# Performance work log

Hardware: AMD Instinct MI355X
Metric: run time of the kernel (lower is better)

The kernel has to match this reference:

```python
import jax, jax.numpy as jnp
import numpy as np

B, C, H, W = 8, 512, 32, 32
HEADS = 8
GROUPS = 32
EPS = 1e-5


def setup_inputs() -> dict:
    key = jax.random.key(0)
    ks = jax.random.split(key, 7)
    x = jax.random.normal(ks[0], (B, C, H, W), dtype=jnp.float32)
    gamma = jnp.ones((C,), dtype=jnp.float32)
    beta = jnp.zeros((C,), dtype=jnp.float32)
    w_qkv = jax.random.normal(ks[1], (3 * C, C), dtype=jnp.float32) * 0.02
    b_qkv = jnp.zeros((3 * C,), dtype=jnp.float32)
    # NOTE: original zero-inits proj; we use small random weights so the
    # attention path contributes to the output (zero proj => out == x).
    w_proj = jax.random.normal(ks[2], (C, C), dtype=jnp.float32) * 0.02
    b_proj = jnp.zeros((C,), dtype=jnp.float32)
    return {"x": x, "gamma": gamma, "beta": beta, "w_qkv": w_qkv,
            "b_qkv": b_qkv, "w_proj": w_proj, "b_proj": b_proj}


def group_norm(x, gamma, beta):
    b, c, h, w = x.shape
    xg = x.reshape(b, GROUPS, -1)
    mu = xg.mean(axis=-1, keepdims=True)
    var = xg.var(axis=-1, keepdims=True)
    xn = ((xg - mu) * jax.lax.rsqrt(var + EPS)).reshape(b, c, h, w)
    return xn * gamma[:, None, None] + beta[:, None, None]


def reference(x, gamma, beta, w_qkv, b_qkv, w_proj, b_proj):
    b, c, h, w = x.shape
    hd = c // HEADS
    n = h * w
    hn = group_norm(x, gamma, beta).reshape(b, c, n)        # [B,C,N]
    # 1x1 conv == channel matmul
    qkv = jnp.einsum('oc,bcn->bon', w_qkv, hn) + b_qkv[:, None]
    qkv = qkv.reshape(b, 3, HEADS, hd, n)
    q, k, v = qkv[:, 0], qkv[:, 1], qkv[:, 2]               # [B,H,hd,N]
    scale = hd ** -0.5
    scores = jnp.einsum('bhci,bhcj->bhij', q, k) * scale    # [B,H,N,N]
    attn = jax.nn.softmax(scores, axis=-1)                  # stable (max-sub)
    out = jnp.einsum('bhij,bhcj->bhci', attn, v).reshape(b, c, n)
    proj = jnp.einsum('oc,bcn->bon', w_proj, out) + b_proj[:, None]
    return x + proj.reshape(b, c, h, w)
```

## Files before the change

### kernel.cpp

```cpp
#include <hip/hip_runtime.h>
#include <hip/hip_cooperative_groups.h>
#include <math.h>

namespace cg = cooperative_groups;

#define Bn 8
#define Cc 512
#define HW 1024
#define HEADS 8
#define HD 64
#define GROUPS 32
#define CPG 16
#define EPS 1e-5f

typedef float f32x4 __attribute__((ext_vector_type(4)));
typedef __bf16 bf16x8 __attribute__((ext_vector_type(8)));
typedef __bf16 bf16x4 __attribute__((ext_vector_type(4)));
typedef short s16x4 __attribute__((ext_vector_type(4)));
typedef unsigned u32x2 __attribute__((ext_vector_type(2)));

__device__ __forceinline__ void async16(const __bf16* g, __bf16* l) {
    __builtin_amdgcn_global_load_lds((const __attribute__((address_space(1))) unsigned int*)g,
                                     (__attribute__((address_space(3))) unsigned int*)l, 16, 0, 0);
}

__device__ __forceinline__ f32x4 mfma16(bf16x4 a, bf16x4 b, f32x4 c) {
    return __builtin_amdgcn_mfma_f32_16x16x16bf16_1k(
        __builtin_bit_cast(s16x4, a), __builtin_bit_cast(s16x4, b), c, 0, 0, 0);
}

__device__ __forceinline__ unsigned pk_bf16(float f1, float f0) {
    return __builtin_amdgcn_perm(__builtin_bit_cast(unsigned, f1),
                                 __builtin_bit_cast(unsigned, f0), 0x07060302u);
}

__device__ __forceinline__ void gn_phase(char* smem, int blk, int tid,
    const float* __restrict__ x, const float* __restrict__ gamma,
    const float* __restrict__ beta, __bf16* __restrict__ hnT,
    const float* __restrict__ wq, __bf16* __restrict__ wq_bf,
    const float* __restrict__ wp, __bf16* __restrict__ wp_bf) {
    if (blk >= 256) {
        int base = (blk - 256) * 512 + tid;
        #pragma unroll
        for (int u = 0; u < 2; ++u) {
            int i = base + u * 256;
            if (i < 196608) {
                float4 v = ((const float4*)wq)[i];
                bf16x4 o = { (__bf16)v.x, (__bf16)v.y, (__bf16)v.z, (__bf16)v.w };
                ((bf16x4*)wq_bf)[i] = o;
            } else {
                int j = i - 196608;
                float4 v = ((const float4*)wp)[j];
                bf16x4 o = { (__bf16)v.x, (__bf16)v.y, (__bf16)v.z, (__bf16)v.w };
                ((bf16x4*)wp_bf)[j] = o;
            }
        }
        return;
    }
    __bf16* xs = (__bf16*)smem;
    float* fs = (float*)smem;
    int b = blk >> 5, g = blk & 31;
    const float* xp = x + ((size_t)b * Cc + g * CPG) * HW;

    float s = 0.f, ss = 0.f;
    for (int i4 = tid; i4 < 4096; i4 += 256) {
        float4 v = ((const float4*)xp)[i4];
        s  += (v.x + v.y) + (v.z + v.w);
        ss += (v.x * v.x + v.y * v.y) + (v.z * v.z + v.w * v.w);
        bf16x4 o = { (__bf16)v.x, (__bf16)v.y, (__bf16)v.z, (__bf16)v.w };
        ((bf16x4*)xs)[i4] = o;
    }
    for (int off = 32; off > 0; off >>= 1) {
        s  += __shfl_down(s, off);
        ss += __shfl_down(ss, off);
    }
    int wave = tid >> 6, lane = tid & 63;
    __syncthreads();
    float keep = 0.f;
    if (tid < 20) keep = (float)xs[tid];
    __syncthreads();
    if (lane == 0) { fs[wave * 2] = s; fs[wave * 2 + 1] = ss; }
    __syncthreads();
    if (tid == 0) {
        float S  = fs[0] + fs[2] + fs[4] + fs[6];
        float SS = fs[1] + fs[3] + fs[5] + fs[7];
        float mean = S / 16384.f;
        float var  = SS / 16384.f - mean * mean;
        fs[8] = mean;
        fs[9] = rsqrtf(var + EPS);
    }
    __syncthreads();
    float mean = fs[8], rstd = fs[9];
    __syncthreads();
    if (tid < 20) xs[tid] = (__bf16)keep;
    __syncthreads();

    float gl[16], bl[16];
    #pragma unroll
    for (int c = 0; c < 16; ++c) { gl[c] = gamma[g * CPG + c]; bl[c] = beta[g * CPG + c]; }
    #pragma unroll
    for (int u = 0; u < 4; ++u) {
        int n = tid + u * 256;
        union { __bf16 bs[16]; uint4 q[2]; } o;
        #pragma unroll
        for (int c = 0; c < 16; ++c) {
            float v = (float)xs[c * 1024 + n];
            o.bs[c] = (__bf16)((v - mean) * rstd * gl[c] + bl[c]);
        }
        uint4* dst = (uint4*)(hnT + ((size_t)b * HW + n) * Cc + g * CPG);
        dst[0] = o.q[0];
        dst[1] = o.q[1];
    }
}

__device__ __forceinline__ void qkv_tile(char* smem, int t, int tid,
    const __bf16* __restrict__ hnT, const __bf16* __restrict__ wq,
    const float* __restrict__ bias, __bf16* __restrict__ qkT,
    __bf16* __restrict__ vbuf, float scaleLo) {
    __bf16* As = (__bf16*)smem;
    __bf16* Bs = (__bf16*)(smem + 16384);
    int wv = tid >> 6, lane = tid & 63, ln = lane & 15, quad = lane >> 4;
    int b = t / 96, rem = t % 96;
    int y = rem >> 3, xv = rem & 7;
    bool isQK = y < 8;
    int bm = (isQK ? y : y - 8) * 128;
    int bn = xv * 128;
    const __bf16* hb = hnT + (size_t)b * HW * Cc;
    const __bf16* Pb = isQK ? hb : wq + (size_t)1024 * 512;
    const __bf16* Qb = isQK ? wq : hb;
    int wm = (wv >> 1) * 64, wn = (wv & 1) * 64;

    f32x4 acc[4][4];
    #pragma unroll
    for (int i = 0; i < 4; ++i)
        #pragma unroll
        for (int j = 0; j < 4; ++j) acc[i][j] = (f32x4){0.f, 0.f, 0.f, 0.f};

    for (int k0 = 0; k0 < 512; k0 += 64) {
        __syncthreads();
        #pragma unroll
        for (int u = 0; u < 4; ++u) {
            int idx = u * 256 + tid;
            int r = idx >> 3, lc = idx & 7;
            int cg2 = lc ^ (r & 7);
            async16(Pb + (size_t)(bm + r) * 512 + k0 + cg2 * 8, &As[r * 64 + lc * 8]);
            async16(Qb + (size_t)(bn + r) * 512 + k0 + cg2 * 8, &Bs[r * 64 + lc * 8]);
        }
        __syncthreads();
        bf16x8 af[4][2], bff[4][2];
        #pragma unroll
        for (int mt = 0; mt < 4; ++mt) {
            int row = wm + mt * 16 + ln;
            #pragma unroll
            for (int h = 0; h < 2; ++h) {
                int cc = (h * 4 + quad) ^ (ln & 7);
                af[mt][h] = *(const bf16x8*)&As[row * 64 + cc * 8];
            }
        }
        #pragma unroll
        for (int nt = 0; nt < 4; ++nt) {
            int row = wn + nt * 16 + ln;
            #pragma unroll
            for (int h = 0; h < 2; ++h) {
                int cc = (h * 4 + quad) ^ (ln & 7);
                bff[nt][h] = *(const bf16x8*)&Bs[row * 64 + cc * 8];
            }
        }
        #pragma unroll
        for (int mt = 0; mt < 4; ++mt)
            #pragma unroll
            for (int nt = 0; nt < 4; ++nt) {
                acc[mt][nt] = __builtin_amdgcn_mfma_f32_16x16x32_bf16(af[mt][0], bff[nt][0], acc[mt][nt], 0, 0, 0);
                acc[mt][nt] = __builtin_amdgcn_mfma_f32_16x16x32_bf16(af[mt][1], bff[nt][1], acc[mt][nt], 0, 0, 0);
            }
    }

    if (isQK) {
        __bf16* out = qkT + (size_t)b * HW * 1024;
        float bcol[4], scol[4];
        #pragma unroll
        for (int nt = 0; nt < 4; ++nt) {
            int col = bn + wn + nt * 16 + ln;
            bcol[nt] = bias[col];
            scol[nt] = (col < 512) ? scaleLo : 1.0f;
        }
        #pragma unroll
        for (int mt = 0; mt < 4; ++mt)
            #pragma unroll
            for (int r = 0; r < 4; ++r) {
                int row = bm + wm + mt * 16 + quad * 4 + r;
                #pragma unroll
                for (int nt = 0; nt < 4; ++nt) {
                    int col = bn + wn + nt * 16 + ln;
                    out[(size_t)row * 1024 + col] = (__bf16)((acc[mt][nt][r] + bcol[nt]) * scol[nt]);
                }
            }
    } else {
        __bf16* out = vbuf + (size_t)b * Cc * HW;
        #pragma unroll
        for (int mt = 0; mt < 4; ++mt)
            #pragma unroll
            for (int r = 0; r < 4; ++r) {
                int row = bm + wm + mt * 16 + quad * 4 + r;
                float brow = bias[1024 + row];
                #pragma unroll
                for (int nt = 0; nt < 4; ++nt) {
                    int col = bn + wn + nt * 16 + ln;
                    out[(size_t)row * 1024 + col] = (__bf16)(acc[mt][nt][r] + brow);
                }
            }
    }
}

__device__ __forceinline__ void attn_unit(char* smem, int blk, int tid,
    const __bf16* __restrict__ qkT, const __bf16* __restrict__ vbuf,
    __bf16* __restrict__ attnT) {
    __bf16* Ks = (__bf16*)smem;
    __bf16* Vs = (__bf16*)(smem + 16384);
    int wv = tid >> 6, lane = tid & 63, ln = lane & 15, quad = lane >> 4;
    int h = blk & 7, qb = (blk >> 3) & 7, b = blk >> 6;
    int i0 = qb * 128 + wv * 32;

    const __bf16* qbase = qkT + ((size_t)b * HW + i0 + ln) * 1024 + h * HD + quad * 8;
    bf16x8 qf[2][2];
    #pragma unroll
    for (int mt = 0; mt < 2; ++mt) {
        qf[mt][0] = *(const bf16x8*)(qbase + (size_t)mt * 16 * 1024);
        qf[mt][1] = *(const bf16x8*)(qbase + (size_t)mt * 16 * 1024 + 32);
    }

    f32x4 oacc[2][4];
    #pragma unroll
    for (int mt = 0; mt < 2; ++mt)
        #pragma unroll
        for (int ct = 0; ct < 4; ++ct) oacc[mt][ct] = (f32x4){0.f, 0.f, 0.f, 0.f};
    float lsum[2] = {0.f, 0.f};

    for (int kt = 0; kt < 8; ++kt) {
        __syncthreads();
        #pragma unroll
        for (int hh = 0; hh < 2; ++hh) {
            int kb = kt * 128 + hh * 64;
            #pragma unroll
            for (int u = 0; u < 2; ++u) {
                int idx = u * 256 + tid;
                int r = idx >> 3, lc = idx & 7;
                int cg2 = lc ^ (r & 7);
                async16(qkT + ((size_t)b * HW + kb + r) * 1024 + 512 + h * HD + cg2 * 8,
                        &Ks[hh * 4096 + idx * 8]);
                async16(vbuf + ((size_t)b * Cc + h * HD + r) * HW + kb + cg2 * 8,
                        &Vs[hh * 4096 + idx * 8]);
            }
        }
        __syncthreads();

        #pragma unroll
        for (int hh = 0; hh < 2; ++hh) {
            f32x4 st[2][4];
            #pragma unroll
            for (int jt = 0; jt < 4; ++jt) {
                int row = jt * 16 + ln;
                int c0 = quad ^ (ln & 7);
                int c1 = (4 + quad) ^ (ln & 7);
                bf16x8 kf0 = *(const bf16x8*)&Ks[hh * 4096 + row * 64 + c0 * 8];
                bf16x8 kf1 = *(const bf16x8*)&Ks[hh * 4096 + row * 64 + c1 * 8];
                #pragma unroll
                for (int mt = 0; mt < 2; ++mt) {
                    f32x4 s = (f32x4){0.f, 0.f, 0.f, 0.f};
                    s = __builtin_amdgcn_mfma_f32_16x16x32_bf16(kf0, qf[mt][0], s, 0, 0, 0);
                    s = __builtin_amdgcn_mfma_f32_16x16x32_bf16(kf1, qf[mt][1], s, 0, 0, 0);
                    st[mt][jt] = s;
                }
            }

            bf16x4 pk[2][4];
            #pragma unroll
            for (int mt = 0; mt < 2; ++mt)
                #pragma unroll
                for (int jt = 0; jt < 4; ++jt) {
                    float p0 = __builtin_amdgcn_exp2f(st[mt][jt][0]);
                    float p1 = __builtin_amdgcn_exp2f(st[mt][jt][1]);
                    float p2 = __builtin_amdgcn_exp2f(st[mt][jt][2]);
                    float p3 = __builtin_amdgcn_exp2f(st[mt][jt][3]);
                    lsum[mt] += (p0 + p1) + (p2 + p3);
                    u32x2 w = { pk_bf16(p1, p0), pk_bf16(p3, p2) };
                    pk[mt][jt] = __builtin_bit_cast(bf16x4, w);
                }

            #pragma unroll
            for (int ct = 0; ct < 4; ++ct) {
                int row = ct * 16 + ln;
                bf16x4 vf[4];
                #pragma unroll
                for (int kss = 0; kss < 4; ++kss) {
                    int cc16 = (kss * 2 + (quad >> 1)) ^ (ln & 7);
                    vf[kss] = *(const bf16x4*)&Vs[hh * 4096 + row * 64 + cc16 * 8 + (quad & 1) * 4];
                }
                #pragma unroll
                for (int mt = 0; mt < 2; ++mt)
                    #pragma unroll
                    for (int kss = 0; kss < 4; ++kss)
                        oacc[mt][ct] = mfma16(vf[kss], pk[mt][kss], oacc[mt][ct]);
            }
        }
    }

    #pragma unroll
    for (int mt = 0; mt < 2; ++mt) {
        lsum[mt] += __shfl_xor(lsum[mt], 16);
        lsum[mt] += __shfl_xor(lsum[mt], 32);
        float rl = 1.f / lsum[mt];
        __bf16* op = attnT + ((size_t)b * HW + i0 + mt * 16 + ln) * Cc + h * HD + quad * 4;
        #pragma unroll
        for (int ct = 0; ct < 4; ++ct) {
            bf16x4 o = { (__bf16)(oacc[mt][ct][0] * rl), (__bf16)(oacc[mt][ct][1] * rl),
                         (__bf16)(oacc[mt][ct][2] * rl), (__bf16)(oacc[mt][ct][3] * rl) };
            *(bf16x4*)(op + ct * 16) = o;
        }
    }
}

__device__ __forceinline__ void proj_unit(char* smem, int blk, int tid,
    const __bf16* __restrict__ wp, const __bf16* __restrict__ attnT,
    const float* __restrict__ bias, const float* __restrict__ resid,
    float* __restrict__ outp) {
    __bf16* As = (__bf16*)smem;
    __bf16* Bs = (__bf16*)(smem + 8192);
    int wv = tid >> 6, lane = tid & 63, ln = lane & 15, quad = lane >> 4;
    int xv = blk & 7, y = (blk >> 3) & 7, b = blk >> 6;
    int bm = y * 64, bn = xv * 128;
    const __bf16* Qb = attnT + (size_t)b * HW * Cc;
    int wm = (wv >> 1) * 32, wn = (wv & 1) * 64;

    f32x4 acc[2][4];
    #pragma unroll
    for (int i = 0; i < 2; ++i)
        #pragma unroll
        for (int j = 0; j < 4; ++j) acc[i][j] = (f32x4){0.f, 0.f, 0.f, 0.f};

    for (int k0 = 0; k0 < 512; k0 += 64) {
        __syncthreads();
        #pragma unroll
        for (int u = 0; u < 2; ++u) {
            int idx = u * 256 + tid;
            int r = idx >> 3, lc = idx & 7;
            int cg2 = lc ^ (r & 7);
            async16(wp + (size_t)(bm + r) * 512 + k0 + cg2 * 8, &As[r * 64 + lc * 8]);
        }
        #pragma unroll
        for (int u = 0; u < 4; ++u) {
            int idx = u * 256 + tid;
            int r = idx >> 3, lc = idx & 7;
            int cg2 = lc ^ (r & 7);
            async16(Qb + (size_t)(bn + r) * 512 + k0 + cg2 * 8, &Bs[r * 64 + lc * 8]);
        }
        __syncthreads();
        bf16x8 af[2][2], bff[4][2];
        #pragma unroll
        for (int mt = 0; mt < 2; ++mt) {
            int row = wm + mt * 16 + ln;
            #pragma unroll
            for (int h = 0; h < 2; ++h) {
                int cc = (h * 4 + quad) ^ (ln & 7);
                af[mt][h] = *(const bf16x8*)&As[row * 64 + cc * 8];
            }
        }
        #pragma unroll
        for (int nt = 0; nt < 4; ++nt) {
            int row = wn + nt * 16 + ln;
            #pragma unroll
            for (int h = 0; h < 2; ++h) {
                int cc = (h * 4 + quad) ^ (ln & 7);
                bff[nt][h] = *(const bf16x8*)&Bs[row * 64 + cc * 8];
            }
        }
        #pragma unroll
        for (int mt = 0; mt < 2; ++mt)
            #pragma unroll
            for (int nt = 0; nt < 4; ++nt) {
                acc[mt][nt] = __builtin_amdgcn_mfma_f32_16x16x32_bf16(af[mt][0], bff[nt][0], acc[mt][nt], 0, 0, 0);
                acc[mt][nt] = __builtin_amdgcn_mfma_f32_16x16x32_bf16(af[mt][1], bff[nt][1], acc[mt][nt], 0, 0, 0);
            }
    }

    float* out = outp + (size_t)b * Cc * HW;
    const float* res = resid + (size_t)b * Cc * HW;
    #pragma unroll
    for (int mt = 0; mt < 2; ++mt)
        #pragma unroll
        for (int r = 0; r < 4; ++r) {
            int row = bm + wm + mt * 16 + quad * 4 + r;
            float bv = bias[row];
            #pragma unroll
            for (int nt = 0; nt < 4; ++nt) {
                int col = bn + wn + nt * 16 + ln;
                size_t idx = (size_t)row * 1024 + col;
                out[idx] = acc[mt][nt][r] + bv + res[idx];
            }
        }
}

__global__ __launch_bounds__(256, 3) void mega(
    const float* __restrict__ x, const float* __restrict__ gamma,
    const float* __restrict__ beta,
    const float* __restrict__ wq_f, const float* __restrict__ wp_f,
    const float* __restrict__ bq, const float* __restrict__ bp,
    __bf16* wq_bf, __bf16* wp_bf, __bf16* hnT, __bf16* qkT,
    __bf16* vbuf, __bf16* attnT, float* out, float qscale) {
    __shared__ __align__(16) char smem[32768];
    int blk = blockIdx.x, tid = threadIdx.x;
    cg::grid_group grid = cg::this_grid();

    gn_phase(smem, blk, tid, x, gamma, beta, hnT, wq_f, wq_bf, wp_f, wp_bf);
    grid.sync();
    qkv_tile(smem, blk, tid, hnT, wq_bf, bq, qkT, vbuf, qscale);
    grid.sync();
    if (blk < 512) attn_unit(smem, blk, tid, qkT, vbuf, attnT);
    grid.sync();
    if (blk < 512) proj_unit(smem, blk, tid, wp_bf, attnT, bp, x, out);
}

__global__ __launch_bounds__(256, 3) void gn_k(
    const float* x, const float* gamma, const float* beta, __bf16* hnT,
    const float* wq, __bf16* wq_bf, const float* wp, __bf16* wp_bf) {
    __shared__ __align__(16) char smem[32768];
    gn_phase(smem, blockIdx.x, threadIdx.x, x, gamma, beta, hnT, wq, wq_bf, wp, wp_bf);
}
__global__ __launch_bounds__(256, 3) void qkv_k(
    const __bf16* hnT, const __bf16* wq, const float* bq,
    __bf16* qkT, __bf16* vbuf, float qscale) {
    __shared__ __align__(16) char smem[32768];
    qkv_tile(smem, blockIdx.x, threadIdx.x, hnT, wq, bq, qkT, vbuf, qscale);
}
__global__ __launch_bounds__(256, 3) void attn_k(
    const __bf16* qkT, const __bf16* vbuf, __bf16* attnT) {
    __shared__ __align__(16) char smem[32768];
    attn_unit(smem, blockIdx.x, threadIdx.x, qkT, vbuf, attnT);
}
__global__ __launch_bounds__(256, 3) void proj_k(
    const __bf16* wp, const __bf16* attnT, const float* bp,
    const float* resid, float* out) {
    __shared__ __align__(16) char smem[32768];
    proj_unit(smem, blockIdx.x, threadIdx.x, wp, attnT, bp, resid, out);
}

extern "C" void kernel_launch(void* const* d_in, const int* in_sizes, int n_in,
                              void* d_out, int out_size, void* d_ws, size_t ws_size,
                              hipStream_t stream) {
    const float* x      = (const float*)d_in[0];
    const float* gamma  = (const float*)d_in[1];
    const float* beta   = (const float*)d_in[2];
    const float* w_qkv  = (const float*)d_in[3];
    const float* b_qkv  = (const float*)d_in[4];
    const float* w_proj = (const float*)d_in[5];
    const float* b_proj = (const float*)d_in[6];
    float* out = (float*)d_out;

    __bf16* wq_bf  = (__bf16*)d_ws;
    __bf16* wp_bf  = wq_bf + (size_t)1536 * 512;
    __bf16* hnT    = wp_bf + (size_t)512 * 512;
    __bf16* qkT    = hnT + (size_t)Bn * HW * Cc;
    __bf16* vbuf   = qkT + (size_t)Bn * HW * 1024;
    __bf16* attnT  = vbuf + (size_t)Bn * Cc * HW;

    float qscale = 0.125f * 1.44269504088896f;

    gn_k<<<768, 256, 0, stream>>>(x, gamma, beta, hnT, w_qkv, wq_bf, w_proj, wp_bf);
    qkv_k<<<768, 256, 0, stream>>>(hnT, wq_bf, b_qkv, qkT, vbuf, qscale);
    attn_k<<<512, 256, 0, stream>>>(qkT, vbuf, attnT);
    proj_k<<<512, 256, 0, stream>>>(wp_bf, attnT, b_proj, x, out);
}
```

Measured before the change: 141.3 us.

## Double-buffer LDS tiles in qkv, attention and projection kernels; drop cooperative mega kernel

Adds a two-stage LDS ping-pong to the qkv, attention and projection loops. The async global-to-LDS copy of the next K tile is issued before the MFMA work on the current tile, which should hide load latency and halves the barriers per iteration. Shared memory per block doubles (64KB/48KB) and launch bounds drop to 2 blocks per CU, trading occupancy for overlap. The unused cooperative mega kernel is removed.

```diff
diff --git a/kernel.cpp b/kernel.cpp
--- a/kernel.cpp
+++ b/kernel.cpp
@@ -1,8 +1,5 @@
 #include <hip/hip_runtime.h>
-#include <hip/hip_cooperative_groups.h>
 #include <math.h>
-
-namespace cg = cooperative_groups;
 
 #define Bn 8
 #define Cc 512
@@ -113,12 +110,25 @@
     }
 }
 
+__device__ __forceinline__ void qkv_stage(char* base, int tid,
+    const __bf16* __restrict__ Pb, const __bf16* __restrict__ Qb,
+    int bm, int bn, int k0) {
+    __bf16* As = (__bf16*)base;
+    __bf16* Bs = (__bf16*)(base + 16384);
+    #pragma unroll
+    for (int u = 0; u < 4; ++u) {
+        int idx = u * 256 + tid;
+        int r = idx >> 3, lc = idx & 7;
+        int cg2 = lc ^ (r & 7);
+        async16(Pb + (size_t)(bm + r) * 512 + k0 + cg2 * 8, &As[idx * 8]);
+        async16(Qb + (size_t)(bn + r) * 512 + k0 + cg2 * 8, &Bs[idx * 8]);
+    }
+}
+
 __device__ __forceinline__ void qkv_tile(char* smem, int t, int tid,
     const __bf16* __restrict__ hnT, const __bf16* __restrict__ wq,
     const float* __restrict__ bias, __bf16* __restrict__ qkT,
     __bf16* __restrict__ vbuf, float scaleLo) {
-    __bf16* As = (__bf16*)smem;
-    __bf16* Bs = (__bf16*)(smem + 16384);
     int wv = tid >> 6, lane = tid & 63, ln = lane & 15, quad = lane >> 4;
     int b = t / 96, rem = t % 96;
     int y = rem >> 3, xv = rem & 7;
@@ -136,17 +146,16 @@
         #pragma unroll
         for (int j = 0; j < 4; ++j) acc[i][j] = (f32x4){0.f, 0.f, 0.f, 0.f};
 
-    for (int k0 = 0; k0 < 512; k0 += 64) {
-        __syncthreads();
-        #pragma unroll
-        for (int u = 0; u < 4; ++u) {
-            int idx = u * 256 + tid;
-            int r = idx >> 3, lc = idx & 7;
-            int cg2 = lc ^ (r & 7);
-            async16(Pb + (size_t)(bm + r) * 512 + k0 + cg2 * 8, &As[r * 64 + lc * 8]);
-            async16(Qb + (size_t)(bn + r) * 512 + k0 + cg2 * 8, &Bs[r * 64 + lc * 8]);
-        }
-        __syncthreads();
+    char* sm_cur = smem;
+    char* sm_nxt = smem + 32768;
+
+    qkv_stage(sm_cur, tid, Pb, Qb, bm, bn, 0);
+    __syncthreads();
+
+    for (int kt = 0; kt < 8; ++kt) {
+        if (kt < 7) qkv_stage(sm_nxt, tid, Pb, Qb, bm, bn, (kt + 1) * 64);
+        __bf16* As = (__bf16*)sm_cur;
+        __bf16* Bs = (__bf16*)(sm_cur + 16384);
         bf16x8 af[4][2], bff[4][2];
         #pragma unroll
         for (int mt = 0; mt < 4; ++mt) {
@@ -173,6 +182,8 @@
                 acc[mt][nt] = __builtin_amdgcn_mfma_f32_16x16x32_bf16(af[mt][0], bff[nt][0], acc[mt][nt], 0, 0, 0);
                 acc[mt][nt] = __builtin_amdgcn_mfma_f32_16x16x32_bf16(af[mt][1], bff[nt][1], acc[mt][nt], 0, 0, 0);
             }
+        __syncthreads();
+        char* tmp = sm_cur; sm_cur = sm_nxt; sm_nxt = tmp;
     }
 
     if (isQK) {
@@ -212,11 +223,30 @@
     }
 }
 
+__device__ __forceinline__ void attn_stage(char* base, int tid,
+    const __bf16* __restrict__ qkT, const __bf16* __restrict__ vbuf,
+    int b, int h, int kt) {
+    __bf16* Ks = (__bf16*)base;
+    __bf16* Vs = (__bf16*)(base + 16384);
+    #pragma unroll
+    for (int hh = 0; hh < 2; ++hh) {
+        int kb = kt * 128 + hh * 64;
+        #pragma unroll
+        for (int u = 0; u < 2; ++u) {
+            int idx = u * 256 + tid;
+            int r = idx >> 3, lc = idx & 7;
+            int cg2 = lc ^ (r & 7);
+            async16(qkT + ((size_t)b * HW + kb + r) * 1024 + 512 + h * HD + cg2 * 8,
+                    &Ks[hh * 4096 + idx * 8]);
+            async16(vbuf + ((size_t)b * Cc + h * HD + r) * HW + kb + cg2 * 8,
+                    &Vs[hh * 4096 + idx * 8]);
+        }
+    }
+}
+
 __device__ __forceinline__ void attn_unit(char* smem, int blk, int tid,
     const __bf16* __restrict__ qkT, const __bf16* __restrict__ vbuf,
     __bf16* __restrict__ attnT) {
-    __bf16* Ks = (__bf16*)smem;
-    __bf16* Vs = (__bf16*)(smem + 16384);
     int wv = tid >> 6, lane = tid & 63, ln = lane & 15, quad = lane >> 4;
     int h = blk & 7, qb = (blk >> 3) & 7, b = blk >> 6;
     int i0 = qb * 128 + wv * 32;
@@ -236,23 +266,15 @@
         for (int ct = 0; ct < 4; ++ct) oacc[mt][ct] = (f32x4){0.f, 0.f, 0.f, 0.f};
     float lsum[2] = {0.f, 0.f};
 
+    char* sm_cur = smem;
+    char* sm_nxt = smem + 32768;
+    attn_stage(sm_cur, tid, qkT, vbuf, b, h, 0);
+    __syncthreads();
+
     for (int kt = 0; kt < 8; ++kt) {
-        __syncthreads();
-        #pragma unroll
-        for (int hh = 0; hh < 2; ++hh) {
-            int kb = kt * 128 + hh * 64;
-            #pragma unroll
-            for (int u = 0; u < 2; ++u) {
-                int idx = u * 256 + tid;
-                int r = idx >> 3, lc = idx & 7;
-                int cg2 = lc ^ (r & 7);
-                async16(qkT + ((size_t)b * HW + kb + r) * 1024 + 512 + h * HD + cg2 * 8,
-                        &Ks[hh * 4096 + idx * 8]);
-                async16(vbuf + ((size_t)b * Cc + h * HD + r) * HW + kb + cg2 * 8,
-                        &Vs[hh * 4096 + idx * 8]);
-            }
-        }
-        __syncthreads();
+        if (kt < 7) attn_stage(sm_nxt, tid, qkT, vbuf, b, h, kt + 1);
+        __bf16* Ks = (__bf16*)sm_cur;
+        __bf16* Vs = (__bf16*)(sm_cur + 16384);
 
         #pragma unroll
         for (int hh = 0; hh < 2; ++hh) {
@@ -303,6 +325,8 @@
                         oacc[mt][ct] = mfma16(vf[kss], pk[mt][kss], oacc[mt][ct]);
             }
         }
+        __syncthreads();
+        char* tmp = sm_cur; sm_cur = sm_nxt; sm_nxt = tmp;
     }
 
     #pragma unroll
@@ -320,12 +344,31 @@
     }
 }
 
+__device__ __forceinline__ void proj_stage(char* base, int tid,
+    const __bf16* __restrict__ wp, const __bf16* __restrict__ Qb,
+    int bm, int bn, int k0) {
+    __bf16* As = (__bf16*)base;
+    __bf16* Bs = (__bf16*)(base + 8192);
+    #pragma unroll
+    for (int u = 0; u < 2; ++u) {
+        int idx = u * 256 + tid;
+        int r = idx >> 3, lc = idx & 7;
+        int cg2 = lc ^ (r & 7);
+        async16(wp + (size_t)(bm + r) * 512 + k0 + cg2 * 8, &As[idx * 8]);
+    }
+    #pragma unroll
+    for (int u = 0; u < 4; ++u) {
+        int idx = u * 256 + tid;
+        int r = idx >> 3, lc = idx & 7;
+        int cg2 = lc ^ (r & 7);
+        async16(Qb + (size_t)(bn + r) * 512 + k0 + cg2 * 8, &Bs[idx * 8]);
+    }
+}
+
 __device__ __forceinline__ void proj_unit(char* smem, int blk, int tid,
     const __bf16* __restrict__ wp, const __bf16* __restrict__ attnT,
     const float* __restrict__ bias, const float* __restrict__ resid,
     float* __restrict__ outp) {
-    __bf16* As = (__bf16*)smem;
-    __bf16* Bs = (__bf16*)(smem + 8192);
     int wv = tid >> 6, lane = tid & 63, ln = lane & 15, quad = lane >> 4;
     int xv = blk & 7, y = (blk >> 3) & 7, b = blk >> 6;
     int bm = y * 64, bn = xv * 128;
@@ -338,23 +381,15 @@
         #pragma unroll
         for (int j = 0; j < 4; ++j) acc[i][j] = (f32x4){0.f, 0.f, 0.f, 0.f};
 
-    for (int k0 = 0; k0 < 512; k0 += 64) {
-        __syncthreads();
-        #pragma unroll
-        for (int u = 0; u < 2; ++u) {
-            int idx = u * 256 + tid;
-            int r = idx >> 3, lc = idx & 7;
-            int cg2 = lc ^ (r & 7);
-            async16(wp + (size_t)(bm + r) * 512 + k0 + cg2 * 8, &As[r * 64 + lc * 8]);
-        }
-        #pragma unroll
-        for (int u = 0; u < 4; ++u) {
-            int idx = u * 256 + tid;
-            int r = idx >> 3, lc = idx & 7;
-            int cg2 = lc ^ (r & 7);
-            async16(Qb + (size_t)(bn + r) * 512 + k0 + cg2 * 8, &Bs[r * 64 + lc * 8]);
-        }
-        __syncthreads();
+    char* sm_cur = smem;
+    char* sm_nxt = smem + 24576;
+    proj_stage(sm_cur, tid, wp, Qb, bm, bn, 0);
+    __syncthreads();
+
+    for (int kt = 0; kt < 8; ++kt) {
+        if (kt < 7) proj_stage(sm_nxt, tid, wp, Qb, bm, bn, (kt + 1) * 64);
+        __bf16* As = (__bf16*)sm_cur;
+        __bf16* Bs = (__bf16*)(sm_cur + 8192);
         bf16x8 af[2][2], bff[4][2];
         #pragma unroll
         for (int mt = 0; mt < 2; ++mt) {
@@ -381,6 +416,8 @@
                 acc[mt][nt] = __builtin_amdgcn_mfma_f32_16x16x32_bf16(af[mt][0], bff[nt][0], acc[mt][nt], 0, 0, 0);
                 acc[mt][nt] = __builtin_amdgcn_mfma_f32_16x16x32_bf16(af[mt][1], bff[nt][1], acc[mt][nt], 0, 0, 0);
             }
+        __syncthreads();
+        char* tmp = sm_cur; sm_cur = sm_nxt; sm_nxt = tmp;
     }
 
     float* out = outp + (size_t)b * Cc * HW;
@@ -398,26 +435,6 @@
                 out[idx] = acc[mt][nt][r] + bv + res[idx];
             }
         }
-}
-
-__global__ __launch_bounds__(256, 3) void mega(
-    const float* __restrict__ x, const float* __restrict__ gamma,
-    const float* __restrict__ beta,
-    const float* __restrict__ wq_f, const float* __restrict__ wp_f,
-    const float* __restrict__ bq, const float* __restrict__ bp,
-    __bf16* wq_bf, __bf16* wp_bf, __bf16* hnT, __bf16* qkT,
-    __bf16* vbuf, __bf16* attnT, float* out, float qscale) {
-    __shared__ __align__(16) char smem[32768];
-    int blk = blockIdx.x, tid = threadIdx.x;
-    cg::grid_group grid = cg::this_grid();
-
-    gn_phase(smem, blk, tid, x, gamma, beta, hnT, wq_f, wq_bf, wp_f, wp_bf);
-    grid.sync();
-    qkv_tile(smem, blk, tid, hnT, wq_bf, bq, qkT, vbuf, qscale);
-    grid.sync();
-    if (blk < 512) attn_unit(smem, blk, tid, qkT, vbuf, attnT);
-    grid.sync();
-    if (blk < 512) proj_unit(smem, blk, tid, wp_bf, attnT, bp, x, out);
 }
 
 __global__ __launch_bounds__(256, 3) void gn_k(
@@ -426,21 +443,21 @@
     __shared__ __align__(16) char smem[32768];
     gn_phase(smem, blockIdx.x, threadIdx.x, x, gamma, beta, hnT, wq, wq_bf, wp, wp_bf);
 }
-__global__ __launch_bounds__(256, 3) void qkv_k(
+__global__ __launch_bounds__(256, 2) void qkv_k(
     const __bf16* hnT, const __bf16* wq, const float* bq,
     __bf16* qkT, __bf16* vbuf, float qscale) {
-    __shared__ __align__(16) char smem[32768];
+    __shared__ __align__(16) char smem[65536];
     qkv_tile(smem, blockIdx.x, threadIdx.x, hnT, wq, bq, qkT, vbuf, qscale);
 }
-__global__ __launch_bounds__(256, 3) void attn_k(
+__global__ __launch_bounds__(256, 2) void attn_k(
     const __bf16* qkT, const __bf16* vbuf, __bf16* attnT) {
-    __shared__ __align__(16) char smem[32768];
+    __shared__ __align__(16) char smem[65536];
     attn_unit(smem, blockIdx.x, threadIdx.x, qkT, vbuf, attnT);
 }
-__global__ __launch_bounds__(256, 3) void proj_k(
+__global__ __launch_bounds__(256, 2) void proj_k(
     const __bf16* wp, const __bf16* attnT, const float* bp,
     const float* resid, float* out) {
-    __shared__ __align__(16) char smem[32768];
+    __shared__ __align__(16) char smem[49152];
     proj_unit(smem, blockIdx.x, threadIdx.x, wp, attnT, bp, resid, out);
 }
 
```

Measured after the change: 141.0 us. Within noise of the previous version (-0.3%).

## Load GEMM and attention operands straight from global memory, bypassing LDS staging

Applied to the files above, without the earlier changes.

Removes the shared-memory staging and block barriers from the QKV, attention and projection kernels. Each wave now reads its MFMA fragments directly from global memory through the cache. The unused cooperative mega-kernel is deleted, and launch bounds for the attention and projection kernels drop from 3 to 2 waves-per-EU hints. This cuts LDS traffic and syncs but loses cross-wave operand sharing, so global/L2 traffic per block rises and loads become less coalesced.

```diff
diff --git a/kernel.cpp b/kernel.cpp
--- a/kernel.cpp
+++ b/kernel.cpp
@@ -1,8 +1,5 @@
 #include <hip/hip_runtime.h>
-#include <hip/hip_cooperative_groups.h>
 #include <math.h>
-
-namespace cg = cooperative_groups;
 
 #define Bn 8
 #define Cc 512
@@ -18,11 +15,6 @@
 typedef __bf16 bf16x4 __attribute__((ext_vector_type(4)));
 typedef short s16x4 __attribute__((ext_vector_type(4)));
 typedef unsigned u32x2 __attribute__((ext_vector_type(2)));
-
-__device__ __forceinline__ void async16(const __bf16* g, __bf16* l) {
-    __builtin_amdgcn_global_load_lds((const __attribute__((address_space(1))) unsigned int*)g,
-                                     (__attribute__((address_space(3))) unsigned int*)l, 16, 0, 0);
-}
 
 __device__ __forceinline__ f32x4 mfma16(bf16x4 a, bf16x4 b, f32x4 c) {
     return __builtin_amdgcn_mfma_f32_16x16x16bf16_1k(
@@ -113,12 +105,10 @@
     }
 }
 
-__device__ __forceinline__ void qkv_tile(char* smem, int t, int tid,
+__device__ __forceinline__ void qkv_tile(int t, int tid,
     const __bf16* __restrict__ hnT, const __bf16* __restrict__ wq,
     const float* __restrict__ bias, __bf16* __restrict__ qkT,
     __bf16* __restrict__ vbuf, float scaleLo) {
-    __bf16* As = (__bf16*)smem;
-    __bf16* Bs = (__bf16*)(smem + 16384);
     int wv = tid >> 6, lane = tid & 63, ln = lane & 15, quad = lane >> 4;
     int b = t / 96, rem = t % 96;
     int y = rem >> 3, xv = rem & 7;
@@ -136,36 +126,22 @@
         #pragma unroll
         for (int j = 0; j < 4; ++j) acc[i][j] = (f32x4){0.f, 0.f, 0.f, 0.f};
 
+    const __bf16* arow = Pb + (size_t)(bm + wm + ln) * 512 + quad * 8;
+    const __bf16* brow = Qb + (size_t)(bn + wn + ln) * 512 + quad * 8;
+
+    #pragma unroll
     for (int k0 = 0; k0 < 512; k0 += 64) {
-        __syncthreads();
-        #pragma unroll
-        for (int u = 0; u < 4; ++u) {
-            int idx = u * 256 + tid;
-            int r = idx >> 3, lc = idx & 7;
-            int cg2 = lc ^ (r & 7);
-            async16(Pb + (size_t)(bm + r) * 512 + k0 + cg2 * 8, &As[r * 64 + lc * 8]);
-            async16(Qb + (size_t)(bn + r) * 512 + k0 + cg2 * 8, &Bs[r * 64 + lc * 8]);
-        }
-        __syncthreads();
         bf16x8 af[4][2], bff[4][2];
         #pragma unroll
-        for (int mt = 0; mt < 4; ++mt) {
-            int row = wm + mt * 16 + ln;
-            #pragma unroll
-            for (int h = 0; h < 2; ++h) {
-                int cc = (h * 4 + quad) ^ (ln & 7);
-                af[mt][h] = *(const bf16x8*)&As[row * 64 + cc * 8];
-            }
-        }
-        #pragma unroll
-        for (int nt = 0; nt < 4; ++nt) {
-            int row = wn + nt * 16 + ln;
-            #pragma unroll
-            for (int h = 0; h < 2; ++h) {
-                int cc = (h * 4 + quad) ^ (ln & 7);
-                bff[nt][h] = *(const bf16x8*)&Bs[row * 64 + cc * 8];
-            }
-        }
+        for (int mt = 0; mt < 4; ++mt)
+            #pragma unroll
+            for (int h = 0; h < 2; ++h)
+                af[mt][h] = *(const bf16x8*)(arow + mt * 16 * 512 + k0 + h * 32);
+        #pragma unroll
+        for (int nt = 0; nt < 4; ++nt)
+            #pragma unroll
+            for (int h = 0; h < 2; ++h)
+                bff[nt][h] = *(const bf16x8*)(brow + nt * 16 * 512 + k0 + h * 32);
         #pragma unroll
         for (int mt = 0; mt < 4; ++mt)
             #pragma unroll
@@ -212,11 +188,9 @@
     }
 }
 
-__device__ __forceinline__ void attn_unit(char* smem, int blk, int tid,
+__device__ __forceinline__ void attn_unit(int blk, int tid,
     const __bf16* __restrict__ qkT, const __bf16* __restrict__ vbuf,
     __bf16* __restrict__ attnT) {
-    __bf16* Ks = (__bf16*)smem;
-    __bf16* Vs = (__bf16*)(smem + 16384);
     int wv = tid >> 6, lane = tid & 63, ln = lane & 15, quad = lane >> 4;
     int h = blk & 7, qb = (blk >> 3) & 7, b = blk >> 6;
     int i0 = qb * 128 + wv * 32;
@@ -229,6 +203,9 @@
         qf[mt][1] = *(const bf16x8*)(qbase + (size_t)mt * 16 * 1024 + 32);
     }
 
+    const __bf16* kbase = qkT + ((size_t)b * HW + ln) * 1024 + 512 + h * HD + quad * 8;
+    const __bf16* vbase = vbuf + ((size_t)b * Cc + h * HD + ln) * HW + (quad & 1) * 4;
+
     f32x4 oacc[2][4];
     #pragma unroll
     for (int mt = 0; mt < 2; ++mt)
@@ -236,34 +213,17 @@
         for (int ct = 0; ct < 4; ++ct) oacc[mt][ct] = (f32x4){0.f, 0.f, 0.f, 0.f};
     float lsum[2] = {0.f, 0.f};
 
+    #pragma unroll 2
     for (int kt = 0; kt < 8; ++kt) {
-        __syncthreads();
         #pragma unroll
         for (int hh = 0; hh < 2; ++hh) {
             int kb = kt * 128 + hh * 64;
-            #pragma unroll
-            for (int u = 0; u < 2; ++u) {
-                int idx = u * 256 + tid;
-                int r = idx >> 3, lc = idx & 7;
-                int cg2 = lc ^ (r & 7);
-                async16(qkT + ((size_t)b * HW + kb + r) * 1024 + 512 + h * HD + cg2 * 8,
-                        &Ks[hh * 4096 + idx * 8]);
-                async16(vbuf + ((size_t)b * Cc + h * HD + r) * HW + kb + cg2 * 8,
-                        &Vs[hh * 4096 + idx * 8]);
-            }
-        }
-        __syncthreads();
-
-        #pragma unroll
-        for (int hh = 0; hh < 2; ++hh) {
             f32x4 st[2][4];
             #pragma unroll
             for (int jt = 0; jt < 4; ++jt) {
-                int row = jt * 16 + ln;
-                int c0 = quad ^ (ln & 7);
-                int c1 = (4 + quad) ^ (ln & 7);
-                bf16x8 kf0 = *(const bf16x8*)&Ks[hh * 4096 + row * 64 + c0 * 8];
-                bf16x8 kf1 = *(const bf16x8*)&Ks[hh * 4096 + row * 64 + c1 * 8];
+                const __bf16* kp = kbase + (size_t)(kb + jt * 16) * 1024;
+                bf16x8 kf0 = *(const bf16x8*)kp;
+                bf16x8 kf1 = *(const bf16x8*)(kp + 32);
                 #pragma unroll
                 for (int mt = 0; mt < 2; ++mt) {
                     f32x4 s = (f32x4){0.f, 0.f, 0.f, 0.f};
@@ -289,13 +249,11 @@
 
             #pragma unroll
             for (int ct = 0; ct < 4; ++ct) {
-                int row = ct * 16 + ln;
                 bf16x4 vf[4];
                 #pragma unroll
-                for (int kss = 0; kss < 4; ++kss) {
-                    int cc16 = (kss * 2 + (quad >> 1)) ^ (ln & 7);
-                    vf[kss] = *(const bf16x4*)&Vs[hh * 4096 + row * 64 + cc16 * 8 + (quad & 1) * 4];
-                }
+                for (int kss = 0; kss < 4; ++kss)
+                    vf[kss] = *(const bf16x4*)(vbase + (size_t)(ct * 16) * HW + kb +
+                                               (kss * 2 + (quad >> 1)) * 8);
                 #pragma unroll
                 for (int mt = 0; mt < 2; ++mt)
                     #pragma unroll
@@ -320,12 +278,10 @@
     }
 }
 
-__device__ __forceinline__ void proj_unit(char* smem, int blk, int tid,
+__device__ __forceinline__ void proj_unit(int blk, int tid,
     const __bf16* __restrict__ wp, const __bf16* __restrict__ attnT,
     const float* __restrict__ bias, const float* __restrict__ resid,
     float* __restrict__ outp) {
-    __bf16* As = (__bf16*)smem;
-    __bf16* Bs = (__bf16*)(smem + 8192);
     int wv = tid >> 6, lane = tid & 63, ln = lane & 15, quad = lane >> 4;
     int xv = blk & 7, y = (blk >> 3) & 7, b = blk >> 6;
     int bm = y * 64, bn = xv * 128;
@@ -338,42 +294,22 @@
         #pragma unroll
         for (int j = 0; j < 4; ++j) acc[i][j] = (f32x4){0.f, 0.f, 0.f, 0.f};
 
+    const __bf16* arow = wp + (size_t)(bm + wm + ln) * 512 + quad * 8;
+    const __bf16* brow = Qb + (size_t)(bn + wn + ln) * 512 + quad * 8;
+
+    #pragma unroll
     for (int k0 = 0; k0 < 512; k0 += 64) {
-        __syncthreads();
-        #pragma unroll
-        for (int u = 0; u < 2; ++u) {
-            int idx = u * 256 + tid;
-            int r = idx >> 3, lc = idx & 7;
-            int cg2 = lc ^ (r & 7);
-            async16(wp + (size_t)(bm + r) * 512 + k0 + cg2 * 8, &As[r * 64 + lc * 8]);
-        }
-        #pragma unroll
-        for (int u = 0; u < 4; ++u) {
-            int idx = u * 256 + tid;
-            int r = idx >> 3, lc = idx & 7;
-            int cg2 = lc ^ (r & 7);
-            async16(Qb + (size_t)(bn + r) * 512 + k0 + cg2 * 8, &Bs[r * 64 + lc * 8]);
-        }
-        __syncthreads();
         bf16x8 af[2][2], bff[4][2];
         #pragma unroll
-        for (int mt = 0; mt < 2; ++mt) {
-            int row = wm + mt * 16 + ln;
-            #pragma unroll
-            for (int h = 0; h < 2; ++h) {
-                int cc = (h * 4 + quad) ^ (ln & 7);
-                af[mt][h] = *(const bf16x8*)&As[row * 64 + cc * 8];
-            }
-        }
-        #pragma unroll
-        for (int nt = 0; nt < 4; ++nt) {
-            int row = wn + nt * 16 + ln;
-            #pragma unroll
-            for (int h = 0; h < 2; ++h) {
-                int cc = (h * 4 + quad) ^ (ln & 7);
-                bff[nt][h] = *(const bf16x8*)&Bs[row * 64 + cc * 8];
-            }
-        }
+        for (int mt = 0; mt < 2; ++mt)
+            #pragma unroll
+            for (int h = 0; h < 2; ++h)
+                af[mt][h] = *(const bf16x8*)(arow + mt * 16 * 512 + k0 + h * 32);
+        #pragma unroll
+        for (int nt = 0; nt < 4; ++nt)
+            #pragma unroll
+            for (int h = 0; h < 2; ++h)
+                bff[nt][h] = *(const bf16x8*)(brow + nt * 16 * 512 + k0 + h * 32);
         #pragma unroll
         for (int mt = 0; mt < 2; ++mt)
             #pragma unroll
@@ -398,26 +334,6 @@
                 out[idx] = acc[mt][nt][r] + bv + res[idx];
             }
         }
-}
-
-__global__ __launch_bounds__(256, 3) void mega(
-    const float* __restrict__ x, const float* __restrict__ gamma,
-    const float* __restrict__ beta,
-    const float* __restrict__ wq_f, const float* __restrict__ wp_f,
-    const float* __restrict__ bq, const float* __restrict__ bp,
-    __bf16* wq_bf, __bf16* wp_bf, __bf16* hnT, __bf16* qkT,
-    __bf16* vbuf, __bf16* attnT, float* out, float qscale) {
-    __shared__ __align__(16) char smem[32768];
-    int blk = blockIdx.x, tid = threadIdx.x;
-    cg::grid_group grid = cg::this_grid();
-
-    gn_phase(smem, blk, tid, x, gamma, beta, hnT, wq_f, wq_bf, wp_f, wp_bf);
-    grid.sync();
-    qkv_tile(smem, blk, tid, hnT, wq_bf, bq, qkT, vbuf, qscale);
-    grid.sync();
-    if (blk < 512) attn_unit(smem, blk, tid, qkT, vbuf, attnT);
-    grid.sync();
-    if (blk < 512) proj_unit(smem, blk, tid, wp_bf, attnT, bp, x, out);
 }
 
 __global__ __launch_bounds__(256, 3) void gn_k(
@@ -429,19 +345,16 @@
 __global__ __launch_bounds__(256, 3) void qkv_k(
     const __bf16* hnT, const __bf16* wq, const float* bq,
     __bf16* qkT, __bf16* vbuf, float qscale) {
-    __shared__ __align__(16) char smem[32768];
-    qkv_tile(smem, blockIdx.x, threadIdx.x, hnT, wq, bq, qkT, vbuf, qscale);
-}
-__global__ __launch_bounds__(256, 3) void attn_k(
+    qkv_tile(blockIdx.x, threadIdx.x, hnT, wq, bq, qkT, vbuf, qscale);
+}
+__global__ __launch_bounds__(256, 2) void attn_k(
     const __bf16* qkT, const __bf16* vbuf, __bf16* attnT) {
-    __shared__ __align__(16) char smem[32768];
-    attn_unit(smem, blockIdx.x, threadIdx.x, qkT, vbuf, attnT);
-}
-__global__ __launch_bounds__(256, 3) void proj_k(
+    attn_unit(blockIdx.x, threadIdx.x, qkT, vbuf, attnT);
+}
+__global__ __launch_bounds__(256, 2) void proj_k(
     const __bf16* wp, const __bf16* attnT, const float* bp,
     const float* resid, float* out) {
-    __shared__ __align__(16) char smem[32768];
-    proj_unit(smem, blockIdx.x, threadIdx.x, wp, attnT, bp, resid, out);
+    proj_unit(blockIdx.x, threadIdx.x, wp, attnT, bp, resid, out);
 }
 
 extern "C" void kernel_launch(void* const* d_in, const int* in_sizes, int n_in,
```

Result: slower. 267.4 us (+89.2%).
